# Optimization experiments

Measured on AMD Instinct MI355X. Metric: run time of the kernel, lower is better.

Reference implementation:

```python
import jax, jax.numpy as jnp
import numpy as np

B, N, D = 4, 2048, 1024
H = 16
DH = D // H  # 64
SCALE = DH ** -0.5


def setup_inputs() -> dict:
    key = jax.random.key(0)
    k1, k2, k3 = jax.random.split(key, 3)
    x = jax.random.normal(k1, (B, N, D), dtype=jnp.float32)
    W_qkv = jax.random.normal(k2, (D, 3 * D), dtype=jnp.float32) / np.sqrt(D)
    b_qkv = jnp.zeros((3 * D,), dtype=jnp.float32)
    W_out = jax.random.normal(k3, (D, D), dtype=jnp.float32) / np.sqrt(D)
    b_out = jnp.zeros((D,), dtype=jnp.float32)
    return {"x": x, "W_qkv": W_qkv, "b_qkv": b_qkv, "W_out": W_out, "b_out": b_out}


def reference(x, W_qkv, b_qkv, W_out, b_out):
    b, n, f = x.shape
    # fused QKV projection: [b, n, 3*D] -> [3, b, H, n, DH]
    qkv = (x @ W_qkv + b_qkv).reshape(b, n, 3, H, DH).transpose(2, 0, 3, 1, 4)
    q, k, v = qkv[0], qkv[1], qkv[2]
    # scaled dot-product attention (dropout rate is 0.0 -> identity)
    attn = jnp.einsum("bhqd,bhkd->bhqk", q, k) * SCALE
    attn = jax.nn.softmax(attn, axis=-1)
    out = jnp.einsum("bhqk,bhkd->bhqd", attn, v)  # [b, H, n, DH]
    out = out.transpose(0, 2, 1, 3).reshape(b, n, f)
    return out @ W_out + b_out
```

## Files before the change

kernel.cpp:

```cpp
#include <hip/hip_runtime.h>
#include <hip/hip_bf16.h>

typedef __bf16 bf16x8 __attribute__((ext_vector_type(8)));
typedef float f32x4 __attribute__((ext_vector_type(4)));
typedef unsigned short u16x8 __attribute__((ext_vector_type(8)));
typedef unsigned int u32x4 __attribute__((ext_vector_type(4)));

__device__ inline unsigned short f2bf(float f) {
  __hip_bfloat16 h = __float2bfloat16(f);
  return __builtin_bit_cast(unsigned short, h);
}

__device__ inline f32x4 zero4() {
  f32x4 z;
  #pragma unroll
  for (int i = 0; i < 4; ++i) z[i] = 0.0f;
  return z;
}

__device__ inline float exp2_fast(float x) {
  float r;
  asm("v_exp_f32 %0, %1" : "=v"(r) : "v"(x));
  return r;
}

__device__ inline unsigned int cvtpk(float lo, float hi) {
  unsigned int r;
  asm("v_cvt_pk_bf16_f32 %0, %1, %2" : "=v"(r) : "v"(lo), "v"(hi));
  return r;
}

__device__ inline void gload16(const unsigned short* g, unsigned short* l) {
  __builtin_amdgcn_global_load_lds(
      (const __attribute__((address_space(1))) unsigned int*)g,
      (__attribute__((address_space(3))) unsigned int*)l, 16, 0, 0);
}

#define QSCALE 0.18033688011112042f

__global__ __launch_bounds__(256) void cast_x_kernel(const float* __restrict__ in,
                                                     unsigned short* __restrict__ out, int n4) {
  int i = blockIdx.x * 256 + threadIdx.x;
  if (i < n4) {
    float4 v = ((const float4*)in)[i];
    ushort4 o;
    o.x = f2bf(v.x); o.y = f2bf(v.y); o.z = f2bf(v.z); o.w = f2bf(v.w);
    ((ushort4*)out)[i] = o;
  }
}

__global__ __launch_bounds__(256) void transpose_cast_kernel(const float* __restrict__ in,
                                                             unsigned short* __restrict__ out,
                                                             int R, int C) {
  __shared__ float tile[32][33];
  int c0 = blockIdx.x * 32, r0 = blockIdx.y * 32;
  int tx = threadIdx.x, ty = threadIdx.y;
  #pragma unroll
  for (int i = 0; i < 4; i++)
    tile[ty + i * 8][tx] = in[(size_t)(r0 + ty + i * 8) * C + c0 + tx];
  __syncthreads();
  #pragma unroll
  for (int i = 0; i < 4; i++)
    out[(size_t)(c0 + ty + i * 8) * R + r0 + tx] = f2bf(tile[tx][ty + i * 8]);
}

template <int KDIM>
__device__ inline void gemm_tile(const unsigned short* __restrict__ A,
                                 const unsigned short* __restrict__ BT,
                                 int m0, int n0,
                                 unsigned short* ldsA, unsigned short* ldsB,
                                 f32x4 acc[4][4]) {
  const int t = threadIdx.x;
  const int lane = t & 63;
  const int w = t >> 6;
  const int wm = w >> 1, wn = w & 1;
  const int fr = lane & 15;
  const int fg = lane >> 4;
  const int srow = w * 8 + (lane >> 3);
  const int scol = (lane & 7) * 8;

  #pragma unroll
  for (int m = 0; m < 4; m++)
    #pragma unroll
    for (int n = 0; n < 4; n++) acc[m][n] = zero4();

  for (int kt = 0; kt < KDIM / 64; ++kt) {
    __syncthreads();
    #pragma unroll
    for (int i = 0; i < 4; i++) {
      int row = i * 32 + srow;
      gload16(A + (size_t)(m0 + row) * KDIM + kt * 64 + scol, ldsA + row * 64 + scol);
      gload16(BT + (size_t)(n0 + row) * KDIM + kt * 64 + scol, ldsB + row * 64 + scol);
    }
    __syncthreads();
    #pragma unroll
    for (int ks = 0; ks < 2; ++ks) {
      bf16x8 a[4], b[4];
      #pragma unroll
      for (int m = 0; m < 4; m++)
        a[m] = *(const bf16x8*)(ldsA + (wm * 64 + m * 16 + fr) * 64 + ks * 32 + fg * 8);
      #pragma unroll
      for (int n = 0; n < 4; n++)
        b[n] = *(const bf16x8*)(ldsB + (wn * 64 + n * 16 + fr) * 64 + ks * 32 + fg * 8);
      #pragma unroll
      for (int m = 0; m < 4; m++)
        #pragma unroll
        for (int n = 0; n < 4; n++)
          acc[m][n] = __builtin_amdgcn_mfma_f32_16x16x32_bf16(a[m], b[n], acc[m][n], 0, 0, 0);
    }
  }
}

__global__ __launch_bounds__(256) void gemm_qkv_kernel(const unsigned short* __restrict__ xbf,
                                                       const unsigned short* __restrict__ WqkvT,
                                                       const float* __restrict__ bqkv,
                                                       unsigned short* __restrict__ Qws,
                                                       unsigned short* __restrict__ Kst,
                                                       unsigned short* __restrict__ Vst) {
  __shared__ unsigned short ldsA[128 * 64];
  __shared__ unsigned short ldsB[128 * 64];
  int m0 = blockIdx.y * 128, n0 = blockIdx.x * 128;
  f32x4 acc[4][4];
  gemm_tile<1024>(xbf, WqkvT, m0, n0, ldsA, ldsB, acc);

  const int lane = threadIdx.x & 63;
  const int w = threadIdx.x >> 6;
  const int wm = w >> 1, wn = w & 1;
  const int fr = lane & 15, fg = lane >> 4;
  #pragma unroll
  for (int m = 0; m < 4; m++) {
    #pragma unroll
    for (int n = 0; n < 4; n++) {
      int col = n0 + wn * 64 + n * 16 + fr;
      int s = col >> 10, cc = col & 1023, h = cc >> 6, d = cc & 63;
      float bias = bqkv[col];
      #pragma unroll
      for (int r = 0; r < 4; r++) {
        int row = m0 + wm * 64 + m * 16 + fg * 4 + r;
        int bb = row >> 11, tok = row & 2047;
        int bh = bb * 16 + h;
        float val = acc[m][n][r] + bias;
        if (s == 0) {
          Qws[((size_t)bh * 2048 + tok) * 64 + d] = f2bf(val * QSCALE);
        } else if (s == 1) {
          int kk = tok & 63, tile = tok >> 6;
          int w32 = kk & 31;
          int sg = ((kk >> 5) * 2 + ((w32 >> 2) & 1)) * 16 + ((w32 >> 3) << 2) + (w32 & 3);
          Kst[((size_t)bh * 32 + tile) * 4096 + sg * 64 + (((d >> 3) ^ (sg & 7)) * 8) + (d & 7)] =
              f2bf(val);
        } else {
          int kk = tok & 63, tile = tok >> 6;
          Vst[((size_t)bh * 32 + tile) * 4096 + d * 64 + (((kk >> 3) ^ (d & 7)) * 8) + (kk & 7)] =
              f2bf(val);
        }
      }
    }
  }
}

__global__ __launch_bounds__(256) void attn_kernel(const unsigned short* __restrict__ Qws,
                                                   const unsigned short* __restrict__ Kst,
                                                   const unsigned short* __restrict__ Vst,
                                                   unsigned short* __restrict__ attn_out) {
  __shared__ unsigned short ldsK[2][4096];
  __shared__ unsigned short ldsV[2][4096];
  const int t = threadIdx.x, lane = t & 63, w = t >> 6;
  int bid = blockIdx.x;
  int vid = (bid & 7) * 128 + (bid >> 3);
  const int bh = vid >> 4, qt = vid & 15;
  const int q0 = qt * 128;
  const int fr = lane & 15, fg = lane >> 4, sw = fr & 7;
  const size_t bhbase = (size_t)bh * 2048;

  bf16x8 qf[2][2];
  #pragma unroll
  for (int u = 0; u < 2; u++) {
    const unsigned short* qrow = Qws + (bhbase + q0 + w * 32 + u * 16 + fr) * 64;
    qf[u][0] = *(const bf16x8*)(qrow + fg * 8);
    qf[u][1] = *(const bf16x8*)(qrow + 32 + fg * 8);
  }

  f32x4 lvec[2];
  f32x4 ot[2][4];
  #pragma unroll
  for (int u = 0; u < 2; u++) {
    lvec[u] = zero4();
    #pragma unroll
    for (int dt = 0; dt < 4; dt++) ot[u][dt] = zero4();
  }

  const unsigned short* kbase = Kst + (size_t)bh * 32 * 4096 + w * 1024 + lane * 8;
  const unsigned short* vbase = Vst + (size_t)bh * 32 * 4096 + w * 1024 + lane * 8;
  unsigned short* kl0 = &ldsK[0][0] + w * 1024 + lane * 8;
  unsigned short* vl0 = &ldsV[0][0] + w * 1024 + lane * 8;

  gload16(kbase, kl0);           gload16(kbase + 512, kl0 + 512);
  gload16(vbase, vl0);           gload16(vbase + 512, vl0 + 512);

  for (int tt2 = 0; tt2 < 32; tt2 += 2) {
    #pragma unroll
    for (int half = 0; half < 2; half++) {
      const int tt = tt2 + half;
      __syncthreads();
      if (tt + 1 < 32) {
        const unsigned short* kg = kbase + (size_t)(tt + 1) * 4096;
        const unsigned short* vg = vbase + (size_t)(tt + 1) * 4096;
        unsigned short* kd = (half ? kl0 : kl0 + 4096);
        unsigned short* vd = (half ? vl0 : vl0 + 4096);
        gload16(kg, kd);            gload16(kg + 512, kd + 512);
        gload16(vg, vd);            gload16(vg + 512, vd + 512);
      }
      const unsigned short* Kb = &ldsK[half][0];
      const unsigned short* Vb = &ldsV[half][0];

      f32x4 st[2][4];
      __builtin_amdgcn_s_setprio(1);
      #pragma unroll
      for (int c = 0; c < 4; c++) {
        const unsigned short* krow = Kb + (c * 16 + fr) * 64;
        bf16x8 a0 = *(const bf16x8*)(krow + ((fg ^ sw) * 8));
        bf16x8 a1 = *(const bf16x8*)(krow + (((4 + fg) ^ sw) * 8));
        #pragma unroll
        for (int u = 0; u < 2; u++) {
          st[u][c] = __builtin_amdgcn_mfma_f32_16x16x32_bf16(a0, qf[u][0], zero4(), 0, 0, 0);
          st[u][c] = __builtin_amdgcn_mfma_f32_16x16x32_bf16(a1, qf[u][1], st[u][c], 0, 0, 0);
        }
      }
      __builtin_amdgcn_s_setprio(0);

      u32x4 pb[2][2];
      #pragma unroll
      for (int u = 0; u < 2; u++) {
        #pragma unroll
        for (int c = 0; c < 4; c++) {
          #pragma unroll
          for (int r = 0; r < 4; r++) st[u][c][r] = exp2_fast(st[u][c][r]);
          lvec[u] += st[u][c];
        }
        #pragma unroll
        for (int kc = 0; kc < 2; kc++) {
          u32x4 pv;
          pv[0] = cvtpk(st[u][kc * 2][0], st[u][kc * 2][1]);
          pv[1] = cvtpk(st[u][kc * 2][2], st[u][kc * 2][3]);
          pv[2] = cvtpk(st[u][kc * 2 + 1][0], st[u][kc * 2 + 1][1]);
          pv[3] = cvtpk(st[u][kc * 2 + 1][2], st[u][kc * 2 + 1][3]);
          pb[u][kc] = pv;
        }
      }

      __builtin_amdgcn_s_setprio(1);
      #pragma unroll
      for (int dt = 0; dt < 4; dt++) {
        const unsigned short* vrow = Vb + (dt * 16 + fr) * 64;
        #pragma unroll
        for (int kc = 0; kc < 2; kc++) {
          bf16x8 av = *(const bf16x8*)(vrow + (((kc * 4 + fg) ^ sw) * 8));
          #pragma unroll
          for (int u = 0; u < 2; u++)
            ot[u][dt] = __builtin_amdgcn_mfma_f32_16x16x32_bf16(
                av, __builtin_bit_cast(bf16x8, pb[u][kc]), ot[u][dt], 0, 0, 0);
        }
      }
      __builtin_amdgcn_s_setprio(0);
    }
  }

  const int b = bh >> 4, h = bh & 15;
  #pragma unroll
  for (int u = 0; u < 2; u++) {
    float l = lvec[u][0] + lvec[u][1] + lvec[u][2] + lvec[u][3];
    l += __shfl_xor(l, 16, 64);
    l += __shfl_xor(l, 32, 64);
    float rl = 1.0f / l;
    int q = q0 + w * 32 + u * 16 + fr;
    #pragma unroll
    for (int dt = 0; dt < 4; dt++) {
      ushort4 o;
      o.x = f2bf(ot[u][dt][0] * rl);
      o.y = f2bf(ot[u][dt][1] * rl);
      o.z = f2bf(ot[u][dt][2] * rl);
      o.w = f2bf(ot[u][dt][3] * rl);
      int d = dt * 16 + fg * 4;
      *(ushort4*)(attn_out + ((size_t)b * 2048 + q) * 1024 + h * 64 + d) = o;
    }
  }
}

__global__ __launch_bounds__(256) void gemm_out_kernel(const unsigned short* __restrict__ attn,
                                                       const unsigned short* __restrict__ WoutT,
                                                       const float* __restrict__ bout,
                                                       float* __restrict__ out) {
  __shared__ unsigned short ldsA[128 * 64];
  __shared__ unsigned short ldsB[128 * 64];
  int m0 = blockIdx.y * 128, n0 = blockIdx.x * 128;
  f32x4 acc[4][4];
  gemm_tile<1024>(attn, WoutT, m0, n0, ldsA, ldsB, acc);

  const int lane = threadIdx.x & 63;
  const int w = threadIdx.x >> 6;
  const int wm = w >> 1, wn = w & 1;
  const int fr = lane & 15, fg = lane >> 4;
  #pragma unroll
  for (int m = 0; m < 4; m++) {
    #pragma unroll
    for (int n = 0; n < 4; n++) {
      int col = n0 + wn * 64 + n * 16 + fr;
      float bias = bout[col];
      #pragma unroll
      for (int r = 0; r < 4; r++) {
        int row = m0 + wm * 64 + m * 16 + fg * 4 + r;
        out[(size_t)row * 1024 + col] = acc[m][n][r] + bias;
      }
    }
  }
}

extern "C" void kernel_launch(void* const* d_in, const int* in_sizes, int n_in,
                              void* d_out, int out_size, void* d_ws, size_t ws_size,
                              hipStream_t stream) {
  const float* x = (const float*)d_in[0];
  const float* Wqkv = (const float*)d_in[1];
  const float* bqkv = (const float*)d_in[2];
  const float* Wout = (const float*)d_in[3];
  const float* bout = (const float*)d_in[4];
  float* out = (float*)d_out;

  unsigned short* xbf = (unsigned short*)d_ws;
  unsigned short* wqkvT = xbf + 8388608;
  unsigned short* woutT = wqkvT + 3145728;
  unsigned short* Qws = woutT + 1048576;
  unsigned short* Kst = Qws + 8388608;
  unsigned short* Vst = Kst + 8388608;
  unsigned short* attn = xbf;

  cast_x_kernel<<<8192, 256, 0, stream>>>(x, xbf, 2097152);
  transpose_cast_kernel<<<dim3(96, 32), dim3(32, 8), 0, stream>>>(Wqkv, wqkvT, 1024, 3072);
  transpose_cast_kernel<<<dim3(32, 32), dim3(32, 8), 0, stream>>>(Wout, woutT, 1024, 1024);
  gemm_qkv_kernel<<<dim3(24, 64), 256, 0, stream>>>(xbf, wqkvT, bqkv, Qws, Kst, Vst);
  attn_kernel<<<1024, 256, 0, stream>>>(Qws, Kst, Vst, attn);
  gemm_out_kernel<<<dim3(8, 64), 256, 0, stream>>>(attn, woutT, bout, out);
}
```

Measured before the change: 301.9 us.

## Double-buffer GEMM LDS tiles and XOR-swizzle columns to avoid bank conflicts

The shared GEMM tile routine now uses two LDS buffers, prefetching the next K-slice with direct global-to-LDS loads while MFMAs run on the current one. Explicit vmcnt waits and raw barriers replace the two __syncthreads per iteration. Source columns are XOR-swizzled by row so that fragment reads from LDS spread across banks. LDS use per block doubles to 64 KB, which may lower occupancy, and correctness now depends on the hand-tuned vmcnt count.

```diff
diff --git a/kernel.cpp b/kernel.cpp
--- a/kernel.cpp
+++ b/kernel.cpp
@@ -77,37 +77,58 @@
   const int fr = lane & 15;
   const int fg = lane >> 4;
   const int srow = w * 8 + (lane >> 3);
-  const int scol = (lane & 7) * 8;
+  const int dcol = (lane & 7) * 8;
+  const int scol = ((lane & 7) ^ ((lane >> 3) & 7)) * 8;
+  const int rsw = fr & 7;
 
   #pragma unroll
   for (int m = 0; m < 4; m++)
     #pragma unroll
     for (int n = 0; n < 4; n++) acc[m][n] = zero4();
 
-  for (int kt = 0; kt < KDIM / 64; ++kt) {
-    __syncthreads();
+  auto STAGE = [&](int kt, int buf) {
     #pragma unroll
     for (int i = 0; i < 4; i++) {
       int row = i * 32 + srow;
-      gload16(A + (size_t)(m0 + row) * KDIM + kt * 64 + scol, ldsA + row * 64 + scol);
-      gload16(BT + (size_t)(n0 + row) * KDIM + kt * 64 + scol, ldsB + row * 64 + scol);
-    }
-    __syncthreads();
+      gload16(A + (size_t)(m0 + row) * KDIM + kt * 64 + scol,
+              ldsA + buf * 8192 + row * 64 + dcol);
+      gload16(BT + (size_t)(n0 + row) * KDIM + kt * 64 + scol,
+              ldsB + buf * 8192 + row * 64 + dcol);
+    }
+  };
+
+  STAGE(0, 0);
+  int cur = 0;
+  constexpr int NT = KDIM / 64;
+  for (int kt = 0; kt < NT; ++kt) {
+    if (kt + 1 < NT) {
+      STAGE(kt + 1, cur ^ 1);
+      asm volatile("s_waitcnt vmcnt(8)" ::: "memory");
+    } else {
+      asm volatile("s_waitcnt vmcnt(0)" ::: "memory");
+    }
+    __builtin_amdgcn_s_barrier();
+
+    const unsigned short* La = ldsA + cur * 8192;
+    const unsigned short* Lb = ldsB + cur * 8192;
     #pragma unroll
     for (int ks = 0; ks < 2; ++ks) {
       bf16x8 a[4], b[4];
       #pragma unroll
       for (int m = 0; m < 4; m++)
-        a[m] = *(const bf16x8*)(ldsA + (wm * 64 + m * 16 + fr) * 64 + ks * 32 + fg * 8);
+        a[m] = *(const bf16x8*)(La + (wm * 64 + m * 16 + fr) * 64 + (((ks * 4 + fg) ^ rsw) * 8));
       #pragma unroll
       for (int n = 0; n < 4; n++)
-        b[n] = *(const bf16x8*)(ldsB + (wn * 64 + n * 16 + fr) * 64 + ks * 32 + fg * 8);
+        b[n] = *(const bf16x8*)(Lb + (wn * 64 + n * 16 + fr) * 64 + (((ks * 4 + fg) ^ rsw) * 8));
       #pragma unroll
       for (int m = 0; m < 4; m++)
         #pragma unroll
         for (int n = 0; n < 4; n++)
           acc[m][n] = __builtin_amdgcn_mfma_f32_16x16x32_bf16(a[m], b[n], acc[m][n], 0, 0, 0);
     }
+    asm volatile("" ::: "memory");
+    __builtin_amdgcn_s_barrier();
+    cur ^= 1;
   }
 }
 
@@ -117,8 +138,8 @@
                                                        unsigned short* __restrict__ Qws,
                                                        unsigned short* __restrict__ Kst,
                                                        unsigned short* __restrict__ Vst) {
-  __shared__ unsigned short ldsA[128 * 64];
-  __shared__ unsigned short ldsB[128 * 64];
+  __shared__ unsigned short ldsA[2 * 128 * 64];
+  __shared__ unsigned short ldsB[2 * 128 * 64];
   int m0 = blockIdx.y * 128, n0 = blockIdx.x * 128;
   f32x4 acc[4][4];
   gemm_tile<1024>(xbf, WqkvT, m0, n0, ldsA, ldsB, acc);
@@ -290,8 +311,8 @@
                                                        const unsigned short* __restrict__ WoutT,
                                                        const float* __restrict__ bout,
                                                        float* __restrict__ out) {
-  __shared__ unsigned short ldsA[128 * 64];
-  __shared__ unsigned short ldsB[128 * 64];
+  __shared__ unsigned short ldsA[2 * 128 * 64];
+  __shared__ unsigned short ldsB[2 * 128 * 64];
   int m0 = blockIdx.y * 128, n0 = blockIdx.x * 128;
   f32x4 acc[4][4];
   gemm_tile<1024>(attn, WoutT, m0, n0, ldsA, ldsB, acc);
```

Result: faster. 286.3 us (-5.2%).
